# Kernel optimization log

Measured on AMD Instinct MI355X. Metric: run time of the kernel, lower is better.

Reference implementation:

```python
import jax, jax.numpy as jnp
import numpy as np

N_NODES = 100000
N_EDGES = 3200000
N_FEAT = 512
N_CLASS = 40
HIDDEN = 16


def _agnn(x, src, dst, beta, num_nodes):
    # PyG AGNNConv: cosine-similarity attention, softmax over incoming edges.
    norm = jnp.linalg.norm(x, axis=1, keepdims=True)
    x_norm = x / jnp.maximum(norm, 1e-12)
    # per-edge logits: beta * <x_norm_dst, x_norm_src>
    alpha = beta * jnp.sum(x_norm[dst] * x_norm[src], axis=1)  # [E]
    # segment softmax over destination nodes
    m = jax.ops.segment_max(alpha, dst, num_segments=num_nodes)  # [N]
    e = jnp.exp(alpha - m[dst])
    s = jax.ops.segment_sum(e, dst, num_segments=num_nodes)  # [N]
    w = e / jnp.maximum(s[dst], 1e-16)  # [E]
    # weighted aggregation of source features to destination
    return jax.ops.segment_sum(x[src] * w[:, None], dst, num_segments=num_nodes)


def setup_inputs() -> dict:
    key = jax.random.key(0)
    ks = jax.random.split(key, 7)
    x = jax.random.normal(ks[0], (N_NODES, N_FEAT), dtype=jnp.float32)
    edge_index = jax.random.randint(ks[1], (2, N_EDGES), 0, N_NODES, dtype=jnp.int32)
    lin1_w = jax.random.normal(ks[2], (HIDDEN, N_FEAT), dtype=jnp.float32) * (1.0 / np.sqrt(N_FEAT))
    lin1_b = jax.random.normal(ks[3], (HIDDEN,), dtype=jnp.float32) * 0.01
    beta2 = jnp.ones((1,), dtype=jnp.float32)
    lin2_w = jax.random.normal(ks[4], (N_CLASS, HIDDEN), dtype=jnp.float32) * (1.0 / np.sqrt(HIDDEN))
    lin2_b = jax.random.normal(ks[5], (N_CLASS,), dtype=jnp.float32) * 0.01
    return {"x": x, "edge_index": edge_index, "lin1_w": lin1_w, "lin1_b": lin1_b,
            "beta2": beta2, "lin2_w": lin2_w, "lin2_b": lin2_b}


def reference(x, edge_index, lin1_w, lin1_b, beta2, lin2_w, lin2_b):
    src, dst = edge_index[0], edge_index[1]
    n = x.shape[0]
    # eval mode: dropout is identity
    h = jax.nn.relu(x @ lin1_w.T + lin1_b)          # [N, 16]
    h = _agnn(h, src, dst, jnp.float32(1.0), n)     # prop1: beta fixed at 1
    h = _agnn(h, src, dst, beta2[0], n)             # prop2: learnable beta
    logits = h @ lin2_w.T + lin2_b                  # [N, C]
    return jax.nn.log_softmax(logits, axis=1)
```

## Files before the change

kernel.cpp:

```cpp
#include <hip/hip_runtime.h>

#define N_NODES 100000
#define N_EDGES 3200000
#define N_FEAT  512
#define HID     16
#define N_CLASS 40

#define BSHIFT  9
#define BMASK   ((1 << BSHIFT) - 1)
#define NB      196
#define CAP     18432
#define EPB     4096

#define BIN_BLOCKS  ((N_EDGES + EPB - 1) / EPB)
#define NT          (N_NODES / 16)
#define LIN1_BLOCKS ((NT + 3) / 4)

typedef __attribute__((ext_vector_type(8))) short bf16x8;
typedef __attribute__((ext_vector_type(4))) float f32x4;

__device__ inline short2 split_bf(float v) {
    const unsigned u = __float_as_uint(v);
    const short hi = (short)(u >> 16);
    const float hf = __uint_as_float(u & 0xFFFF0000u);
    const short lo = (short)(__float_as_uint(v - hf) >> 16);
    return make_short2(hi, lo);
}
__device__ inline unsigned short f2bf_rtn(float v) {
    unsigned u = __float_as_uint(v);
    u += 0x7FFFu + ((u >> 16) & 1u);
    return (unsigned short)(u >> 16);
}
__device__ inline float bf2f(unsigned short u) {
    return __uint_as_float(((unsigned)u) << 16);
}

struct BinSmem {
    int hist[NB]; int lofs[NB]; int base[NB]; int rk[NB];
    int buf[256]; int stage[EPB]; unsigned short sbkt[EPB];
};
struct Lin1Smem { short bfH[16 * 64 * 8]; short bfL[16 * 64 * 8]; };

__device__ void bin_body(char* smemraw,
                         const int* __restrict__ src,
                         const int* __restrict__ dst,
                         int* __restrict__ cursor,
                         int* __restrict__ binned) {
    BinSmem& sm = *(BinSmem*)smemraw;
    const int t = threadIdx.x;
    for (int i = t; i < NB; i += 256) { sm.hist[i] = 0; sm.rk[i] = 0; }
    __syncthreads();

    const int e0 = blockIdx.x * EPB;
    int bk[EPB / 256];
    int vv[EPB / 256];
#pragma unroll
    for (int k = 0; k < EPB / 256; k++) {
        const int e = e0 + k * 256 + t;
        if (e < N_EDGES) {
            const int d = dst[e], s = src[e];
            bk[k] = d >> BSHIFT;
            vv[k] = (s << BSHIFT) | (d & BMASK);
            atomicAdd(&sm.hist[bk[k]], 1);
        } else bk[k] = -1;
    }
    __syncthreads();

    {
        const int v = (t < NB) ? sm.hist[t] : 0;
        sm.buf[t] = v; __syncthreads();
        for (int o = 1; o < 256; o <<= 1) {
            const int a = (t >= o) ? sm.buf[t - o] : 0;
            __syncthreads();
            sm.buf[t] += a;
            __syncthreads();
        }
        if (t < NB) sm.lofs[t] = sm.buf[t] - v;
    }
    if (t < NB && sm.hist[t] > 0)
        sm.base[t] = t * CAP + atomicAdd(&cursor[t], sm.hist[t]);

#pragma unroll
    for (int k = 0; k < EPB / 256; k++) {
        if (bk[k] >= 0) {
            const int r = atomicAdd(&sm.rk[bk[k]], 1);
            const int slot = sm.lofs[bk[k]] + r;
            sm.stage[slot] = vv[k];
            sm.sbkt[slot] = (unsigned short)bk[k];
        }
    }
    __syncthreads();

    const int nloc = min(EPB, N_EDGES - e0);
    for (int s2 = t; s2 < nloc; s2 += 256) {
        const int b = sm.sbkt[s2];
        binned[sm.base[b] + (s2 - sm.lofs[b])] = sm.stage[s2];
    }
}

__device__ void lin1_body(char* smemraw, int lblk,
                          const float* __restrict__ x,
                          const float* __restrict__ w1,
                          const float* __restrict__ b1,
                          unsigned short* __restrict__ xnb,
                          float* __restrict__ normv) {
    Lin1Smem& sm = *(Lin1Smem*)smemraw;
    const int t = threadIdx.x;
    for (int f = t; f < 16 * 64; f += 256) {
        const int kt  = f >> 6;
        const int ln  = f & 63;
        const int col = ln & 15;
        const int k0  = kt * 32 + (ln >> 4) * 8;
        const float4 v0 = *(const float4*)(w1 + col * N_FEAT + k0);
        const float4 v1 = *(const float4*)(w1 + col * N_FEAT + k0 + 4);
        bf16x8 hh, ll;
        short2 r;
        r = split_bf(v0.x); hh[0] = r.x; ll[0] = r.y;
        r = split_bf(v0.y); hh[1] = r.x; ll[1] = r.y;
        r = split_bf(v0.z); hh[2] = r.x; ll[2] = r.y;
        r = split_bf(v0.w); hh[3] = r.x; ll[3] = r.y;
        r = split_bf(v1.x); hh[4] = r.x; ll[4] = r.y;
        r = split_bf(v1.y); hh[5] = r.x; ll[5] = r.y;
        r = split_bf(v1.z); hh[6] = r.x; ll[6] = r.y;
        r = split_bf(v1.w); hh[7] = r.x; ll[7] = r.y;
        ((bf16x8*)sm.bfH)[f] = hh;
        ((bf16x8*)sm.bfL)[f] = ll;
    }
    __syncthreads();

    const int wv   = t >> 6;
    const int l    = t & 63;
    const int tile = lblk * 4 + wv;
    if (tile >= NT) return;

    const int r0 = tile * 16;
    const float* xp = x + (size_t)(r0 + (l & 15)) * N_FEAT + ((l >> 4) * 8);

    f32x4 acc = {0.f, 0.f, 0.f, 0.f};
    float4 c0 = *(const float4*)(xp);
    float4 c1 = *(const float4*)(xp + 4);
#pragma unroll
    for (int kt = 0; kt < 16; ++kt) {
        float4 n0, n1;
        if (kt < 15) {
            n0 = *(const float4*)(xp + (kt + 1) * 32);
            n1 = *(const float4*)(xp + (kt + 1) * 32 + 4);
        }
        bf16x8 ah, al;
        short2 r;
        r = split_bf(c0.x); ah[0] = r.x; al[0] = r.y;
        r = split_bf(c0.y); ah[1] = r.x; al[1] = r.y;
        r = split_bf(c0.z); ah[2] = r.x; al[2] = r.y;
        r = split_bf(c0.w); ah[3] = r.x; al[3] = r.y;
        r = split_bf(c1.x); ah[4] = r.x; al[4] = r.y;
        r = split_bf(c1.y); ah[5] = r.x; al[5] = r.y;
        r = split_bf(c1.z); ah[6] = r.x; al[6] = r.y;
        r = split_bf(c1.w); ah[7] = r.x; al[7] = r.y;
        const bf16x8 bh = ((const bf16x8*)sm.bfH)[kt * 64 + l];
        const bf16x8 bl = ((const bf16x8*)sm.bfL)[kt * 64 + l];
        acc = __builtin_amdgcn_mfma_f32_16x16x32_bf16(ah, bh, acc, 0, 0, 0);
        acc = __builtin_amdgcn_mfma_f32_16x16x32_bf16(al, bh, acc, 0, 0, 0);
        acc = __builtin_amdgcn_mfma_f32_16x16x32_bf16(ah, bl, acc, 0, 0, 0);
        c0 = n0; c1 = n1;
    }

    const float bias = b1[l & 15];
#pragma unroll
    for (int r = 0; r < 4; ++r) {
        const float v = fmaxf(acc[r] + bias, 0.f);
        float ss = v * v;
        ss += __shfl_xor(ss, 1); ss += __shfl_xor(ss, 2);
        ss += __shfl_xor(ss, 4); ss += __shfl_xor(ss, 8);
        const float nrm = sqrtf(ss);
        const float rn  = 1.f / fmaxf(nrm, 1e-12f);
        const int row = r0 + (l >> 4) * 4 + r;
        xnb[(size_t)row * HID + (l & 15)] = f2bf_rtn(v * rn);
        if ((l & 15) == 0) normv[row] = nrm;
    }
}

__global__ __launch_bounds__(256) void k_bin_lin1(const int* __restrict__ src,
                                                  const int* __restrict__ dst,
                                                  int* __restrict__ cursor,
                                                  int* __restrict__ binned,
                                                  const float* __restrict__ x,
                                                  const float* __restrict__ w1,
                                                  const float* __restrict__ b1,
                                                  unsigned short* __restrict__ xnb,
                                                  float* __restrict__ normv) {
    __shared__ __align__(16) char smem[sizeof(Lin1Smem) > sizeof(BinSmem)
                                       ? sizeof(Lin1Smem) : sizeof(BinSmem)];
    if (blockIdx.x < BIN_BLOCKS)
        bin_body(smem, src, dst, cursor, binned);
    else
        lin1_body(smem, blockIdx.x - BIN_BLOCKS, x, w1, b1, xnb, normv);
}

__global__ __launch_bounds__(512) void k_csr(const int* __restrict__ cursor,
                                             int* __restrict__ binned,
                                             int* __restrict__ row_start,
                                             unsigned short* __restrict__ row_cnt) {
    __shared__ int cnts[512];
    __shared__ int cur[512];
    __shared__ int buf[512];
    __shared__ int lcsr[CAP];

    const int t = threadIdx.x;
    const int b = blockIdx.x;
    const int s0 = b * CAP;
    const int n = cursor[b];

    cnts[t] = 0;
    __syncthreads();
    for (int i = t; i < n; i += 512)
        atomicAdd(&cnts[binned[s0 + i] & BMASK], 1);
    __syncthreads();

    {
        const int v = cnts[t];
        buf[t] = v; __syncthreads();
        for (int o = 1; o < 512; o <<= 1) {
            const int a = (t >= o) ? buf[t - o] : 0;
            __syncthreads();
            buf[t] += a;
            __syncthreads();
        }
        cur[t] = buf[t] - v;
        const int node = (b << BSHIFT) + t;
        if (node < N_NODES) {
            row_start[node] = s0 + cur[t];
            row_cnt[node]   = (unsigned short)v;
        }
    }
    __syncthreads();

    for (int i = t; i < n; i += 512) {
        const int v = binned[s0 + i];
        const int p = atomicAdd(&cur[v & BMASK], 1);
        lcsr[p] = v >> BSHIFT;
    }
    __syncthreads();

    for (int i = t; i < n; i += 512) binned[s0 + i] = lcsr[i];
}

template <int EMIT_NORMED>
__global__ __launch_bounds__(256) void k_agnn(const int* __restrict__ row_start,
                                              const unsigned short* __restrict__ row_cnt,
                                              const int* __restrict__ csr_src,
                                              const unsigned short* __restrict__ xnb,
                                              const float* __restrict__ normv,
                                              const float* __restrict__ betap,
                                              float* __restrict__ outf,
                                              unsigned short* __restrict__ outb,
                                              float* __restrict__ out_norm) {
    const int l16  = threadIdx.x & 15;
    const int node = (blockIdx.x * 256 + threadIdx.x) >> 4;
    const float beta  = betap ? betap[0] : 1.0f;
    const float shift = fabsf(beta);

    const int rs  = row_start[node];
    const int cnt = row_cnt[node];

    const bf16x8* xd = (const bf16x8*)(xnb + (size_t)node * HID);
    const bf16x8 dlo = xd[0], dhi = xd[1];
    float dd[16];
#pragma unroll
    for (int i = 0; i < 8; i++) {
        dd[i]     = bf2f((unsigned short)dlo[i]);
        dd[i + 8] = bf2f((unsigned short)dhi[i]);
    }

    const unsigned short* colb = xnb + l16;
    float acc0 = 0.f, acc1 = 0.f, sw = 0.f;

    bool ok = (l16 < cnt);
    int sidx = ok ? csr_src[rs + l16] : 0;
    const bf16x8* xs0 = (const bf16x8*)(xnb + (size_t)sidx * HID);
    bf16x8 slo = xs0[0], shi = xs0[1];
    float nj = normv[sidx];

    for (int t = 0; t < cnt; t += 16) {
        const int k2 = t + 16 + l16;
        const bool ok2 = (k2 < cnt);
        const int sidx2 = ok2 ? csr_src[rs + k2] : 0;
        const bf16x8* xs2 = (const bf16x8*)(xnb + (size_t)sidx2 * HID);
        const bf16x8 slo2 = xs2[0], shi2 = xs2[1];
        const float nj2 = normv[sidx2];

        float p0 = 0.f, p1 = 0.f, p2 = 0.f, p3 = 0.f;
#pragma unroll
        for (int i = 0; i < 4; i++) {
            p0 += bf2f((unsigned short)slo[i])     * dd[i];
            p1 += bf2f((unsigned short)slo[i + 4]) * dd[i + 4];
            p2 += bf2f((unsigned short)shi[i])     * dd[i + 8];
            p3 += bf2f((unsigned short)shi[i + 4]) * dd[i + 12];
        }
        const float dot = (p0 + p1) + (p2 + p3);
        const float w = ok ? __expf(beta * dot - shift) : 0.f;

        float ws = w;
        ws += __shfl_xor(ws, 1); ws += __shfl_xor(ws, 2);
        ws += __shfl_xor(ws, 4); ws += __shfl_xor(ws, 8);
        sw += ws;

        const float wn = w * nj;
#pragma unroll
        for (int j = 0; j < 16; j += 2) {
            const float w0 = __shfl(wn, j, 16);
            const int   s0i = __shfl(sidx, j, 16);
            const float w1 = __shfl(wn, j + 1, 16);
            const int   s1i = __shfl(sidx, j + 1, 16);
            acc0 += w0 * bf2f(colb[(size_t)s0i * HID]);
            acc1 += w1 * bf2f(colb[(size_t)s1i * HID]);
        }

        sidx = sidx2; slo = slo2; shi = shi2; nj = nj2; ok = ok2;
    }

    const float v = (acc0 + acc1) / fmaxf(sw, 1e-16f);
    if (EMIT_NORMED) {
        float ss = v * v;
        ss += __shfl_xor(ss, 1); ss += __shfl_xor(ss, 2);
        ss += __shfl_xor(ss, 4); ss += __shfl_xor(ss, 8);
        const float nrm = sqrtf(ss);
        const float rn  = 1.f / fmaxf(nrm, 1e-12f);
        outb[(size_t)node * HID + l16] = f2bf_rtn(v * rn);
        if (l16 == 0) out_norm[node] = nrm;
    } else {
        outf[(size_t)node * HID + l16] = v;
    }
}

__global__ __launch_bounds__(256) void k_lin2(const float* __restrict__ h,
                                              const float* __restrict__ w2,
                                              const float* __restrict__ b2,
                                              float* __restrict__ out) {
    __shared__ float w2s[N_CLASS][HID];
    __shared__ float b2s[N_CLASS];
    for (int i = threadIdx.x; i < N_CLASS * HID; i += 256)
        ((float*)w2s)[i] = w2[i];
    if (threadIdx.x < N_CLASS) b2s[threadIdx.x] = b2[threadIdx.x];
    __syncthreads();

    const int n = blockIdx.x * 256 + threadIdx.x;
    if (n >= N_NODES) return;

    float hv[HID];
    const float4* hr = (const float4*)(h + (size_t)n * HID);
#pragma unroll
    for (int q = 0; q < 4; q++) {
        const float4 v = hr[q];
        hv[q*4+0]=v.x; hv[q*4+1]=v.y; hv[q*4+2]=v.z; hv[q*4+3]=v.w;
    }

    float lg[N_CLASS];
    float m = -3.0e38f;
#pragma unroll
    for (int j = 0; j < N_CLASS; j++) {
        float acc = b2s[j];
#pragma unroll
        for (int k = 0; k < HID; k++) acc += hv[k] * w2s[j][k];
        lg[j] = acc;
        m = fmaxf(m, acc);
    }
    float sum = 0.f;
#pragma unroll
    for (int j = 0; j < N_CLASS; j++) sum += __expf(lg[j] - m);
    const float lse = m + __logf(sum);

    float4* orow = (float4*)(out + (size_t)n * N_CLASS);
#pragma unroll
    for (int q = 0; q < N_CLASS / 4; q++) {
        float4 o;
        o.x = lg[q*4+0] - lse;
        o.y = lg[q*4+1] - lse;
        o.z = lg[q*4+2] - lse;
        o.w = lg[q*4+3] - lse;
        orow[q] = o;
    }
}

extern "C" void kernel_launch(void* const* d_in, const int* in_sizes, int n_in,
                              void* d_out, int out_size, void* d_ws, size_t ws_size,
                              hipStream_t stream) {
    const float* x     = (const float*)d_in[0];
    const int*   ei    = (const int*)  d_in[1];
    const float* w1    = (const float*)d_in[2];
    const float* b1    = (const float*)d_in[3];
    const float* beta2 = (const float*)d_in[4];
    const float* w2    = (const float*)d_in[5];
    const float* b2    = (const float*)d_in[6];
    float* out = (float*)d_out;

    const int* srcp = ei;
    const int* dstp = ei + N_EDGES;

    unsigned short* xnb1 = (unsigned short*)d_ws;
    unsigned short* xnb2 = xnb1 + (size_t)N_NODES * HID;
    float* norm1 = (float*)(xnb2 + (size_t)N_NODES * HID);
    float* norm2 = norm1 + N_NODES;
    float* hF    = norm2 + N_NODES;
    int* row_start = (int*)(hF + (size_t)N_NODES * HID);
    unsigned short* row_cnt = (unsigned short*)(row_start + N_NODES);
    int* cursor = (int*)(row_cnt + N_NODES + (N_NODES & 1));
    int* binned = cursor + NB + 2;

    const int nodeGrid = (N_NODES + 255) / 256;
    const int agnnGrid = N_NODES * HID / 256;

    hipMemsetAsync(cursor, 0, NB * sizeof(int), stream);

    k_bin_lin1<<<BIN_BLOCKS + LIN1_BLOCKS, 256, 0, stream>>>(
        srcp, dstp, cursor, binned, x, w1, b1, xnb1, norm1);

    k_csr<<<NB, 512, 0, stream>>>(cursor, binned, row_start, row_cnt);

    k_agnn<1><<<agnnGrid, 256, 0, stream>>>(row_start, row_cnt, binned, xnb1,
                                            norm1, nullptr, nullptr, xnb2, norm2);
    k_agnn<0><<<agnnGrid, 256, 0, stream>>>(row_start, row_cnt, binned, xnb2,
                                            norm2, beta2, hF, nullptr, nullptr);

    k_lin2<<<nodeGrid, 256, 0, stream>>>(hF, w2, b2, out);
}
```

Measured before the change: 199.1 us.

## Reuse gathered source rows for aggregation and fuse lin2/log-softmax into AGNN

```diff
diff --git a/kernel.cpp b/kernel.cpp
--- a/kernel.cpp
+++ b/kernel.cpp
@@ -244,16 +244,27 @@
     for (int i = t; i < n; i += 512) binned[s0 + i] = lcsr[i];
 }
 
-template <int EMIT_NORMED>
+template <int LAST>
 __global__ __launch_bounds__(256) void k_agnn(const int* __restrict__ row_start,
                                               const unsigned short* __restrict__ row_cnt,
                                               const int* __restrict__ csr_src,
                                               const unsigned short* __restrict__ xnb,
                                               const float* __restrict__ normv,
                                               const float* __restrict__ betap,
-                                              float* __restrict__ outf,
+                                              const float* __restrict__ w2,
+                                              const float* __restrict__ b2,
+                                              float* __restrict__ out,
                                               unsigned short* __restrict__ outb,
                                               float* __restrict__ out_norm) {
+    __shared__ float w2s[N_CLASS][HID + 1];
+    __shared__ float b2s[N_CLASS];
+    if (LAST) {
+        for (int i = threadIdx.x; i < N_CLASS * HID; i += 256)
+            w2s[i / HID][i % HID] = w2[i];
+        if (threadIdx.x < N_CLASS) b2s[threadIdx.x] = b2[threadIdx.x];
+        __syncthreads();
+    }
+
     const int l16  = threadIdx.x & 15;
     const int node = (blockIdx.x * 256 + threadIdx.x) >> 4;
     const float beta  = betap ? betap[0] : 1.0f;
@@ -271,8 +282,10 @@
         dd[i + 8] = bf2f((unsigned short)dhi[i]);
     }
 
-    const unsigned short* colb = xnb + l16;
-    float acc0 = 0.f, acc1 = 0.f, sw = 0.f;
+    float acc[16];
+#pragma unroll
+    for (int i = 0; i < 16; i++) acc[i] = 0.f;
+    float swl = 0.f;
 
     bool ok = (l16 < cnt);
     int sidx = ok ? csr_src[rs + l16] : 0;
@@ -288,38 +301,47 @@
         const bf16x8 slo2 = xs2[0], shi2 = xs2[1];
         const float nj2 = normv[sidx2];
 
+        float sr[16];
+#pragma unroll
+        for (int i = 0; i < 8; i++) {
+            sr[i]     = bf2f((unsigned short)slo[i]);
+            sr[i + 8] = bf2f((unsigned short)shi[i]);
+        }
         float p0 = 0.f, p1 = 0.f, p2 = 0.f, p3 = 0.f;
 #pragma unroll
         for (int i = 0; i < 4; i++) {
-            p0 += bf2f((unsigned short)slo[i])     * dd[i];
-            p1 += bf2f((unsigned short)slo[i + 4]) * dd[i + 4];
-            p2 += bf2f((unsigned short)shi[i])     * dd[i + 8];
-            p3 += bf2f((unsigned short)shi[i + 4]) * dd[i + 12];
+            p0 += sr[i]      * dd[i];
+            p1 += sr[i + 4]  * dd[i + 4];
+            p2 += sr[i + 8]  * dd[i + 8];
+            p3 += sr[i + 12] * dd[i + 12];
         }
         const float dot = (p0 + p1) + (p2 + p3);
         const float w = ok ? __expf(beta * dot - shift) : 0.f;
-
-        float ws = w;
-        ws += __shfl_xor(ws, 1); ws += __shfl_xor(ws, 2);
-        ws += __shfl_xor(ws, 4); ws += __shfl_xor(ws, 8);
-        sw += ws;
-
+        swl += w;
         const float wn = w * nj;
 #pragma unroll
-        for (int j = 0; j < 16; j += 2) {
-            const float w0 = __shfl(wn, j, 16);
-            const int   s0i = __shfl(sidx, j, 16);
-            const float w1 = __shfl(wn, j + 1, 16);
-            const int   s1i = __shfl(sidx, j + 1, 16);
-            acc0 += w0 * bf2f(colb[(size_t)s0i * HID]);
-            acc1 += w1 * bf2f(colb[(size_t)s1i * HID]);
-        }
+        for (int i = 0; i < 16; i++) acc[i] += wn * sr[i];
 
         sidx = sidx2; slo = slo2; shi = shi2; nj = nj2; ok = ok2;
     }
 
-    const float v = (acc0 + acc1) / fmaxf(sw, 1e-16f);
-    if (EMIT_NORMED) {
+#pragma unroll
+    for (int m = 1; m < 16; m <<= 1) {
+#pragma unroll
+        for (int r = 0; r < 16; r += 2 * m) {
+            const float sel  = (l16 & m) ? acc[r] : acc[r + m];
+            const float got  = __shfl_xor(sel, m);
+            const float mine = (l16 & m) ? acc[r + m] : acc[r];
+            acc[r] = mine + got;
+        }
+    }
+    float sw = swl;
+    sw += __shfl_xor(sw, 1); sw += __shfl_xor(sw, 2);
+    sw += __shfl_xor(sw, 4); sw += __shfl_xor(sw, 8);
+
+    const float v = acc[0] / fmaxf(sw, 1e-16f);
+
+    if (!LAST) {
         float ss = v * v;
         ss += __shfl_xor(ss, 1); ss += __shfl_xor(ss, 2);
         ss += __shfl_xor(ss, 4); ss += __shfl_xor(ss, 8);
@@ -328,56 +350,32 @@
         outb[(size_t)node * HID + l16] = f2bf_rtn(v * rn);
         if (l16 == 0) out_norm[node] = nrm;
     } else {
-        outf[(size_t)node * HID + l16] = v;
-    }
-}
-
-__global__ __launch_bounds__(256) void k_lin2(const float* __restrict__ h,
-                                              const float* __restrict__ w2,
-                                              const float* __restrict__ b2,
-                                              float* __restrict__ out) {
-    __shared__ float w2s[N_CLASS][HID];
-    __shared__ float b2s[N_CLASS];
-    for (int i = threadIdx.x; i < N_CLASS * HID; i += 256)
-        ((float*)w2s)[i] = w2[i];
-    if (threadIdx.x < N_CLASS) b2s[threadIdx.x] = b2[threadIdx.x];
-    __syncthreads();
-
-    const int n = blockIdx.x * 256 + threadIdx.x;
-    if (n >= N_NODES) return;
-
-    float hv[HID];
-    const float4* hr = (const float4*)(h + (size_t)n * HID);
-#pragma unroll
-    for (int q = 0; q < 4; q++) {
-        const float4 v = hr[q];
-        hv[q*4+0]=v.x; hv[q*4+1]=v.y; hv[q*4+2]=v.z; hv[q*4+3]=v.w;
-    }
-
-    float lg[N_CLASS];
-    float m = -3.0e38f;
-#pragma unroll
-    for (int j = 0; j < N_CLASS; j++) {
-        float acc = b2s[j];
-#pragma unroll
-        for (int k = 0; k < HID; k++) acc += hv[k] * w2s[j][k];
-        lg[j] = acc;
-        m = fmaxf(m, acc);
-    }
-    float sum = 0.f;
-#pragma unroll
-    for (int j = 0; j < N_CLASS; j++) sum += __expf(lg[j] - m);
-    const float lse = m + __logf(sum);
-
-    float4* orow = (float4*)(out + (size_t)n * N_CLASS);
-#pragma unroll
-    for (int q = 0; q < N_CLASS / 4; q++) {
-        float4 o;
-        o.x = lg[q*4+0] - lse;
-        o.y = lg[q*4+1] - lse;
-        o.z = lg[q*4+2] - lse;
-        o.w = lg[q*4+3] - lse;
-        orow[q] = o;
+        float vv[16];
+#pragma unroll
+        for (int k = 0; k < 16; k++) vv[k] = __shfl(v, k, 16);
+        const int c0 = l16, c1 = l16 + 16, c2 = l16 + 32;
+        float lg0 = b2s[c0], lg1 = b2s[c1];
+        float lg2 = (l16 < 8) ? b2s[c2] : -3.0e38f;
+#pragma unroll
+        for (int k = 0; k < 16; k++) {
+            lg0 += vv[k] * w2s[c0][k];
+            lg1 += vv[k] * w2s[c1][k];
+            if (l16 < 8) lg2 += vv[k] * w2s[c2][k];
+        }
+        float m = fmaxf(lg0, lg1);
+        if (l16 < 8) m = fmaxf(m, lg2);
+        m = fmaxf(m, __shfl_xor(m, 1)); m = fmaxf(m, __shfl_xor(m, 2));
+        m = fmaxf(m, __shfl_xor(m, 4)); m = fmaxf(m, __shfl_xor(m, 8));
+        float s = __expf(lg0 - m) + __expf(lg1 - m)
+                + ((l16 < 8) ? __expf(lg2 - m) : 0.f);
+        s += __shfl_xor(s, 1); s += __shfl_xor(s, 2);
+        s += __shfl_xor(s, 4); s += __shfl_xor(s, 8);
+        const float lse = m + __logf(s);
+
+        float* orow = out + (size_t)node * N_CLASS;
+        orow[c0] = lg0 - lse;
+        orow[c1] = lg1 - lse;
+        if (l16 < 8) orow[c2] = lg2 - lse;
     }
 }
 
@@ -400,13 +398,11 @@
     unsigned short* xnb2 = xnb1 + (size_t)N_NODES * HID;
     float* norm1 = (float*)(xnb2 + (size_t)N_NODES * HID);
     float* norm2 = norm1 + N_NODES;
-    float* hF    = norm2 + N_NODES;
-    int* row_start = (int*)(hF + (size_t)N_NODES * HID);
+    int* row_start = (int*)(norm2 + N_NODES);
     unsigned short* row_cnt = (unsigned short*)(row_start + N_NODES);
     int* cursor = (int*)(row_cnt + N_NODES + (N_NODES & 1));
     int* binned = cursor + NB + 2;
 
-    const int nodeGrid = (N_NODES + 255) / 256;
     const int agnnGrid = N_NODES * HID / 256;
 
     hipMemsetAsync(cursor, 0, NB * sizeof(int), stream);
@@ -416,10 +412,10 @@
 
     k_csr<<<NB, 512, 0, stream>>>(cursor, binned, row_start, row_cnt);
 
-    k_agnn<1><<<agnnGrid, 256, 0, stream>>>(row_start, row_cnt, binned, xnb1,
-                                            norm1, nullptr, nullptr, xnb2, norm2);
-    k_agnn<0><<<agnnGrid, 256, 0, stream>>>(row_start, row_cnt, binned, xnb2,
-                                            norm2, beta2, hF, nullptr, nullptr);
-
-    k_lin2<<<nodeGrid, 256, 0, stream>>>(hF, w2, b2, out);
-}
+    k_agnn<0><<<agnnGrid, 256, 0, stream>>>(row_start, row_cnt, binned, xnb1,
+                                            norm1, nullptr, nullptr, nullptr,
+                                            nullptr, xnb2, norm2);
+    k_agnn<1><<<agnnGrid, 256, 0, stream>>>(row_start, row_cnt, binned, xnb2,
+                                            norm2, beta2, w2, b2,
+                                            out, nullptr, nullptr);
+}
```

Result: no change. 200.0 us (+0.4%).
